# Performance work log

Measured on AMD Instinct MI355X. Metric: run time of the kernel, lower is better.

The kernel has to match this reference:

```python
import jax, jax.numpy as jnp
import numpy as np

IN_DIM = 1024
OUT_DIM = 1024
QK_DIM = OUT_DIM // 4  # 256


def setup_inputs() -> dict:
    key = jax.random.key(0)
    kx, ky, kq, kk, kv = jax.random.split(key, 5)
    B, Sq, Sk = 16, 2048, 2048
    x = jax.random.normal(kx, (B, Sq, IN_DIM), dtype=jnp.float32)
    y = jax.random.normal(ky, (B, Sk, IN_DIM), dtype=jnp.float32)
    s = 1.0 / np.sqrt(IN_DIM)
    Wq = jax.random.normal(kq, (IN_DIM, QK_DIM), dtype=jnp.float32) * s
    Wk = jax.random.normal(kk, (IN_DIM, QK_DIM), dtype=jnp.float32) * s
    Wv = jax.random.normal(kv, (IN_DIM, OUT_DIM), dtype=jnp.float32) * s
    return {"x": x, "y": y, "Wq": Wq, "Wk": Wk, "Wv": Wv}


def reference(x, y, Wq, Wk, Wv):
    # q: [B,Sq,dk], k: [B,Sk,dk]
    q = jnp.einsum("bsd,dk->bsk", x, Wq)
    k = jnp.einsum("btd,dk->btk", y, Wk)
    # NOTE: original scales by out_dim**0.5, not qk dim
    scores = jnp.einsum("bsk,btk->bst", q, k) / jnp.sqrt(jnp.float32(OUT_DIM))
    attn = jax.nn.softmax(scores, axis=-1)
    v = jnp.einsum("btd,de->bte", y, Wv)
    out = jnp.einsum("bst,bte->bse", attn, v)
    return out + x
```

## Files before the change

### kernel.cpp

```cpp
#include <hip/hip_runtime.h>

typedef __attribute__((ext_vector_type(8))) short bf16x8;
typedef __attribute__((ext_vector_type(4))) short s16x4;
typedef __attribute__((ext_vector_type(4))) float f32x4;

#define MFMA16(a,b,c) __builtin_amdgcn_mfma_f32_16x16x32_bf16((a),(b),(c),0,0,0)

__device__ __forceinline__ unsigned short f2bf(float f) {
  unsigned int u = __float_as_uint(f);
  return (unsigned short)((u + 0x7fffu + ((u >> 16) & 1u)) >> 16);
}
__device__ __forceinline__ float bf2f(unsigned short u) {
  return __uint_as_float(((unsigned int)u) << 16);
}

__device__ __forceinline__ void gload16(const void* g, void* l) {
  __builtin_amdgcn_global_load_lds((const __attribute__((address_space(1))) void*)g,
                                   (__attribute__((address_space(3))) void*)l, 16, 0, 0);
}

__global__ __launch_bounds__(256) void cvt_bf16(const float* __restrict__ in,
                                                unsigned short* __restrict__ out, int n8) {
  for (int i = blockIdx.x * 256 + threadIdx.x; i < n8; i += gridDim.x * 256) {
    float4 a = ((const float4*)in)[2 * i];
    float4 b = ((const float4*)in)[2 * i + 1];
    s16x4 p0, p1;
    p0[0] = f2bf(a.x); p0[1] = f2bf(a.y); p0[2] = f2bf(a.z); p0[3] = f2bf(a.w);
    p1[0] = f2bf(b.x); p1[1] = f2bf(b.y); p1[2] = f2bf(b.z); p1[3] = f2bf(b.w);
    ((s16x4*)out)[2 * i] = p0;
    ((s16x4*)out)[2 * i + 1] = p1;
  }
}

__global__ __launch_bounds__(256) void tcvt(const float* __restrict__ W,
                                            unsigned short* __restrict__ Wt, int K, int N) {
  __shared__ float t[32][33];
  const int n0 = blockIdx.x * 32, k0 = blockIdx.y * 32;
  const int c = threadIdx.x & 31, r8 = threadIdx.x >> 5;
#pragma unroll
  for (int p = 0; p < 4; ++p) {
    int r = r8 + p * 8;
    t[r][c] = W[(size_t)(k0 + r) * N + n0 + c];
  }
  __syncthreads();
#pragma unroll
  for (int p = 0; p < 4; ++p) {
    int r = r8 + p * 8;
    Wt[(size_t)(n0 + r) * K + k0 + c] = f2bf(t[c][r]);
  }
}

__global__ __launch_bounds__(256) void proj_gemm(
    const unsigned short* __restrict__ A, const unsigned short* __restrict__ Bt,
    unsigned short* __restrict__ C, int N, float scale)
{
  __shared__ __align__(16) unsigned short As[2][4096];
  __shared__ __align__(16) unsigned short Bs[2][4096];
  const int tid = threadIdx.x, lane = tid & 63, w = tid >> 6;
  const int wr = w >> 1, wc = w & 1;
  const int lrow = lane & 15, lg = lane >> 4;
  const size_t bm = (size_t)blockIdx.x * 128;
  const size_t bn = (size_t)blockIdx.y * 128;
  const int rl = lane >> 2, cq = lane & 3;

  auto stage = [&](int kt, int buf) {
#pragma unroll
    for (int u = 0; u < 2; ++u) {
      int row = w * 32 + u * 16 + rl;
      gload16(A  + (bm + row) * 1024 + kt * 32 + cq * 8, &As[buf][(w * 32 + u * 16) * 32]);
      gload16(Bt + (bn + row) * 1024 + kt * 32 + cq * 8, &Bs[buf][(w * 32 + u * 16) * 32]);
    }
  };

  f32x4 acc[4][4] = {};
  stage(0, 0);
  __syncthreads();

  for (int kt = 0; kt < 32; ++kt) {
    const int cur = kt & 1;
    if (kt + 1 < 32) stage(kt + 1, cur ^ 1);
    bf16x8 af[4], bfr[4];
#pragma unroll
    for (int i = 0; i < 4; ++i)
      af[i] = *(const bf16x8*)&As[cur][(wr * 64 + i * 16 + lrow) * 32 + lg * 8];
#pragma unroll
    for (int j = 0; j < 4; ++j)
      bfr[j] = *(const bf16x8*)&Bs[cur][(wc * 64 + j * 16 + lrow) * 32 + lg * 8];
    __builtin_amdgcn_s_setprio(1);
#pragma unroll
    for (int i = 0; i < 4; ++i)
#pragma unroll
      for (int j = 0; j < 4; ++j)
        acc[i][j] = MFMA16(af[i], bfr[j], acc[i][j]);
    __builtin_amdgcn_s_setprio(0);
    __syncthreads();
  }

  const int orow0 = blockIdx.x * 128 + wr * 64;
  const int ocol0 = blockIdx.y * 128 + wc * 64;
#pragma unroll
  for (int i = 0; i < 4; ++i)
#pragma unroll
    for (int j = 0; j < 4; ++j) {
      int col = ocol0 + j * 16 + lrow;
#pragma unroll
      for (int r = 0; r < 4; ++r) {
        int row = orow0 + i * 16 + lg * 4 + r;
        C[(size_t)row * N + col] = f2bf(acc[i][j][r] * scale);
      }
    }
}

#define SBAR  do { __builtin_amdgcn_s_barrier(); __builtin_amdgcn_sched_barrier(0); } while (0)

template<int NT, int NTIL, int MODE>
__global__ __launch_bounds__(512) void gemm4p(
    const unsigned short* __restrict__ Aall, const unsigned short* __restrict__ Ball,
    size_t abatch, size_t bbatch, int lda, int ldb,
    unsigned short* __restrict__ Cb, int b0, int nb)
{
  __shared__ __align__(16) unsigned short lds[65536];
  const int bid = blockIdx.x;
  const int bloc = bid % nb, tl = bid / nb;
  const int mtile = tl / NTIL, ntile = tl % NTIL;
  const int gb = b0 + bloc;
  const unsigned short* Ag = Aall + (MODE == 0 ? (size_t)gb : (size_t)bloc) * abatch
                                  + (size_t)mtile * 256 * lda;
  const unsigned short* Bg = Ball + (size_t)gb * bbatch + (size_t)ntile * 256 * ldb;

  const int tid = threadIdx.x, lane = tid & 63, w = tid >> 6;
  const int wm = w >> 2, wn = w & 3;
  const int lrow = lane & 15, lg = lane >> 4;
  char* lb = (char*)lds;

  auto stageU = [&](const unsigned short* G, int ld, int kofs, int ubyte) {
#pragma unroll
    for (int i = 0; i < 2; ++i) {
      int c = tid + 512 * i;
      int row = c >> 2, q = c & 3;
      int qs = q ^ ((row >> 1) & 3);
      gload16(G + (size_t)row * ld + kofs + qs * 8, lb + ubyte + c * 16);
    }
  };
  auto rdfrag = [&](int ubyte, int row) -> bf16x8 {
    return *(const bf16x8*)(lb + ubyte + row * 64 + ((lg ^ ((row >> 1) & 3)) << 4));
  };

  f32x4 acc[8][4] = {};
  bf16x8 afA[4], afB[4], bfrA[4], bfrB[4];

  stageU(Ag, lda, 0,  (0 * 2 + 0) * 16384);
  stageU(Bg, ldb, 0,  (1 * 2 + 0) * 16384);
  stageU(Ag, lda, 32, (2 * 2 + 0) * 16384);
  stageU(Bg, ldb, 32, (3 * 2 + 0) * 16384);
  stageU(Ag, lda, 64, (0 * 2 + 1) * 16384);
  stageU(Bg, ldb, 64, (1 * 2 + 1) * 16384);
  asm volatile("s_waitcnt vmcnt(8)" ::: "memory");
  SBAR;
#pragma unroll
  for (int i = 0; i < 4; ++i) afA[i] = rdfrag(0, wm * 128 + i * 16 + lrow);
#pragma unroll
  for (int nf = 0; nf < 4; ++nf) bfrA[nf] = rdfrag(2 * 16384, wn * 64 + nf * 16 + lrow);

  for (int T = 0; T < NT; ++T) {
    const int pc = T & 1, pn = (T + 1) & 1;
    const int a1b = (2 * 2 + pc) * 16384, b1b = (3 * 2 + pc) * 16384;
    const int a0b = (0 * 2 + pc) * 16384;
    const int t1 = (T + 1 < NT) ? T + 1 : 0;
    const int t2 = (T + 2 < NT) ? T + 2 : 0;

#pragma unroll
    for (int i = 0; i < 4; ++i) afB[i] = rdfrag(a0b, wm * 128 + (i + 4) * 16 + lrow);
    stageU(Ag, lda, t1 * 64 + 32, (2 * 2 + pn) * 16384);
    asm volatile("s_waitcnt lgkmcnt(4)" ::: "memory");
    __builtin_amdgcn_sched_barrier(0);
    __builtin_amdgcn_s_setprio(1);
#pragma unroll
    for (int mf = 0; mf < 4; ++mf)
#pragma unroll
      for (int nf = 0; nf < 4; ++nf)
        acc[mf][nf] = MFMA16(afA[mf], bfrA[nf], acc[mf][nf]);
    __builtin_amdgcn_s_setprio(0);
    asm volatile("s_waitcnt vmcnt(6)" ::: "memory");
    SBAR;

#pragma unroll
    for (int i = 0; i < 4; ++i) afA[i] = rdfrag(a1b, wm * 128 + i * 16 + lrow);
#pragma unroll
    for (int nf = 0; nf < 4; ++nf) bfrB[nf] = rdfrag(b1b, wn * 64 + nf * 16 + lrow);
    stageU(Bg, ldb, t1 * 64 + 32, (3 * 2 + pn) * 16384);
    asm volatile("s_waitcnt lgkmcnt(8)" ::: "memory");
    __builtin_amdgcn_sched_barrier(0);
    __builtin_amdgcn_s_setprio(1);
#pragma unroll
    for (int mf = 0; mf < 4; ++mf)
#pragma unroll
      for (int nf = 0; nf < 4; ++nf)
        acc[mf + 4][nf] = MFMA16(afB[mf], bfrA[nf], acc[mf + 4][nf]);
    __builtin_amdgcn_s_setprio(0);
    SBAR;

#pragma unroll
    for (int i = 0; i < 4; ++i) afB[i] = rdfrag(a1b, wm * 128 + (i + 4) * 16 + lrow);
    stageU(Ag, lda, t2 * 64, (0 * 2 + pc) * 16384);
    asm volatile("s_waitcnt lgkmcnt(4)" ::: "memory");
    __builtin_amdgcn_sched_barrier(0);
    __builtin_amdgcn_s_setprio(1);
#pragma unroll
    for (int mf = 0; mf < 4; ++mf)
#pragma unroll
      for (int nf = 0; nf < 4; ++nf)
        acc[mf][nf] = MFMA16(afA[mf], bfrB[nf], acc[mf][nf]);
    __builtin_amdgcn_s_setprio(0);
    asm volatile("s_waitcnt vmcnt(6)" ::: "memory");
    SBAR;

#pragma unroll
    for (int i = 0; i < 4; ++i) afA[i] = rdfrag((0 * 2 + pn) * 16384, wm * 128 + i * 16 + lrow);
#pragma unroll
    for (int nf = 0; nf < 4; ++nf) bfrA[nf] = rdfrag((1 * 2 + pn) * 16384, wn * 64 + nf * 16 + lrow);
    stageU(Bg, ldb, t2 * 64, (1 * 2 + pc) * 16384);
    asm volatile("s_waitcnt lgkmcnt(8)" ::: "memory");
    __builtin_amdgcn_sched_barrier(0);
    __builtin_amdgcn_s_setprio(1);
#pragma unroll
    for (int mf = 0; mf < 4; ++mf)
#pragma unroll
      for (int nf = 0; nf < 4; ++nf)
        acc[mf + 4][nf] = MFMA16(afB[mf], bfrB[nf], acc[mf + 4][nf]);
    __builtin_amdgcn_s_setprio(0);
    SBAR;
  }

  if (MODE == 0) {
    unsigned short* Cp = Cb + (size_t)bloc * 2048 * 2048;
#pragma unroll
    for (int mf = 0; mf < 8; ++mf)
#pragma unroll
      for (int r = 0; r < 4; ++r) {
        int row = mtile * 256 + wm * 128 + mf * 16 + lg * 4 + r;
#pragma unroll
        for (int nf = 0; nf < 4; ++nf) {
          int col = ntile * 256 + wn * 64 + nf * 16 + lrow;
          Cp[(size_t)row * 2048 + col] = f2bf(acc[mf][nf][r]);
        }
      }
  } else {
    unsigned char* C8 = (unsigned char*)Cb;
#pragma unroll
    for (int mf = 0; mf < 8; ++mf) {
      int m0 = mtile * 256 + wm * 128 + mf * 16 + lg * 4;
      int bb = m0 >> 11, t = m0 & 2047;
      int tw = t >> 6, t64 = t & 63;
#pragma unroll
      for (int nf = 0; nf < 4; ++nf) {
        int e = ntile * 256 + wn * 64 + nf * 16 + lrow;
        int eg = e >> 4;
        int pk = 0;
        pk = __builtin_amdgcn_cvt_pk_fp8_f32(acc[mf][nf][0], acc[mf][nf][1], pk, false);
        pk = __builtin_amdgcn_cvt_pk_fp8_f32(acc[mf][nf][2], acc[mf][nf][3], pk, true);
        *(unsigned int*)(C8 + (size_t)bb * 2097152
                            + ((size_t)(eg * 32 + tw)) * 1024 + lrow * 64 + t64)
            = (unsigned int)pk;
      }
    }
  }
}

__global__ __launch_bounds__(256) void softmax_kernel(
    const unsigned short* __restrict__ Sp, unsigned char* __restrict__ Pp) {
  const int row = blockIdx.x * 4 + (threadIdx.x >> 6);
  const int lane = threadIdx.x & 63;
  const unsigned short* rp = Sp + (size_t)row * 2048;
  bf16x8 raw[4];
#pragma unroll
  for (int c = 0; c < 4; ++c) raw[c] = *(const bf16x8*)(rp + c * 512 + lane * 8);
  float v[32];
#pragma unroll
  for (int c = 0; c < 4; ++c)
#pragma unroll
    for (int j = 0; j < 8; ++j) v[c * 8 + j] = bf2f((unsigned short)raw[c][j]);
  float mx = v[0];
#pragma unroll
  for (int j = 1; j < 32; ++j) mx = fmaxf(mx, v[j]);
  mx = fmaxf(mx, __shfl_xor(mx, 1));
  mx = fmaxf(mx, __shfl_xor(mx, 2));
  mx = fmaxf(mx, __shfl_xor(mx, 4));
  mx = fmaxf(mx, __shfl_xor(mx, 8));
  mx = fmaxf(mx, __shfl_xor(mx, 16));
  mx = fmaxf(mx, __shfl_xor(mx, 32));
  float sum = 0.f;
#pragma unroll
  for (int j = 0; j < 32; ++j) { v[j] = __expf(v[j] - mx); sum += v[j]; }
  sum += __shfl_xor(sum, 1);
  sum += __shfl_xor(sum, 2);
  sum += __shfl_xor(sum, 4);
  sum += __shfl_xor(sum, 8);
  sum += __shfl_xor(sum, 16);
  sum += __shfl_xor(sum, 32);
  const float scale = 64.0f / sum;
  unsigned char* rp8 = Pp + (size_t)row * 2048;
#pragma unroll
  for (int c = 0; c < 4; ++c) {
    int lo = 0, hi = 0;
    lo = __builtin_amdgcn_cvt_pk_fp8_f32(v[c * 8 + 0] * scale, v[c * 8 + 1] * scale, lo, false);
    lo = __builtin_amdgcn_cvt_pk_fp8_f32(v[c * 8 + 2] * scale, v[c * 8 + 3] * scale, lo, true);
    hi = __builtin_amdgcn_cvt_pk_fp8_f32(v[c * 8 + 4] * scale, v[c * 8 + 5] * scale, hi, false);
    hi = __builtin_amdgcn_cvt_pk_fp8_f32(v[c * 8 + 6] * scale, v[c * 8 + 7] * scale, hi, true);
    uint2 o; o.x = (unsigned int)lo; o.y = (unsigned int)hi;
    *(uint2*)(rp8 + c * 512 + lane * 8) = o;
  }
}

__global__ __launch_bounds__(512) void pvf8_kernel(
    const unsigned char* __restrict__ Pp,
    const unsigned char* __restrict__ Vp,
    const float* __restrict__ X, float* __restrict__ Out,
    int b0, int nb)
{
  __shared__ __align__(16) unsigned char lds[4][16384];
  const int bloc = blockIdx.x % nb, tl = blockIdx.x / nb;
  const int mtile = tl >> 3, ntile = tl & 7;
  const int gb = b0 + bloc;
  const unsigned char* Ag = Pp + (size_t)bloc * 4194304 + (size_t)mtile * 256 * 2048;
  const unsigned char* Vb = Vp + (size_t)gb * 2097152;
  const int NT = 32;
  const int tid = threadIdx.x, lane = tid & 63, w = tid >> 6;
  const int wm = w >> 2, wn = w & 3;
  const int lrow = lane & 15, lg = lane >> 4;

  auto stageA = [&](int jt) {
    unsigned char* dst = lds[jt & 3];
#pragma unroll
    for (int i = 0; i < 2; ++i) {
      int c = tid + 512 * i; int row = c >> 2; int q = (c & 3) ^ ((row >> 1) & 3);
      gload16(Ag + (size_t)row * 2048 + jt * 64 + q * 16, dst + c * 16);
    }
  };

  f32x4 acc[8][2] = {};
  stageA(0); stageA(1); stageA(2);
  asm volatile("s_waitcnt vmcnt(4)" ::: "memory");

  for (int jt = 0; jt < NT; ++jt) {
    __builtin_amdgcn_s_barrier();
    long2 bv[2];
#pragma unroll
    for (int nf = 0; nf < 2; ++nf) {
      int eg = ntile * 8 + wn * 2 + nf;
      bv[nf] = *(const long2*)(Vb + ((size_t)(eg * 32 + jt)) * 1024 + lrow * 64 + lg * 16);
    }
    if (jt + 3 < NT) stageA(jt + 3);
    const unsigned char* Ab = lds[jt & 3];
    {
      long2 av[4];
#pragma unroll
      for (int mf = 0; mf < 4; ++mf) {
        int row = wm * 128 + mf * 16 + lrow;
        av[mf] = *(const long2*)(Ab + row * 64 + ((lg ^ ((row >> 1) & 3)) << 4));
      }
      __builtin_amdgcn_s_setprio(1);
#pragma unroll
      for (int mf = 0; mf < 4; ++mf)
#pragma unroll
        for (int nf = 0; nf < 2; ++nf) {
          acc[mf][nf] = __builtin_amdgcn_mfma_f32_16x16x32_fp8_fp8(av[mf].x, bv[nf].x, acc[mf][nf], 0, 0, 0);
          acc[mf][nf] = __builtin_amdgcn_mfma_f32_16x16x32_fp8_fp8(av[mf].y, bv[nf].y, acc[mf][nf], 0, 0, 0);
        }
      __builtin_amdgcn_s_setprio(0);
    }
    {
      long2 av[4];
#pragma unroll
      for (int mf = 0; mf < 4; ++mf) {
        int row = wm * 128 + (mf + 4) * 16 + lrow;
        av[mf] = *(const long2*)(Ab + row * 64 + ((lg ^ ((row >> 1) & 3)) << 4));
      }
      __builtin_amdgcn_s_setprio(1);
#pragma unroll
      for (int mf = 0; mf < 4; ++mf)
#pragma unroll
        for (int nf = 0; nf < 2; ++nf) {
          acc[mf + 4][nf] = __builtin_amdgcn_mfma_f32_16x16x32_fp8_fp8(av[mf].x, bv[nf].x, acc[mf + 4][nf], 0, 0, 0);
          acc[mf + 4][nf] = __builtin_amdgcn_mfma_f32_16x16x32_fp8_fp8(av[mf].y, bv[nf].y, acc[mf + 4][nf], 0, 0, 0);
        }
      __builtin_amdgcn_s_setprio(0);
    }
  }

#pragma unroll
  for (int mf = 0; mf < 8; ++mf)
#pragma unroll
    for (int r = 0; r < 4; ++r) {
      int row = mtile * 256 + wm * 128 + mf * 16 + lg * 4 + r;
      const float* xr = X   + ((size_t)gb * 2048 + row) * 1024;
      float*      orp = Out + ((size_t)gb * 2048 + row) * 1024;
#pragma unroll
      for (int nf = 0; nf < 2; ++nf) {
        int col = ntile * 128 + wn * 32 + nf * 16 + lrow;
        orp[col] = acc[mf][nf][r] * 0.015625f + xr[col];
      }
    }
}

extern "C" void kernel_launch(void* const* d_in, const int* in_sizes, int n_in,
                              void* d_out, int out_size, void* d_ws, size_t ws_size,
                              hipStream_t stream) {
  (void)in_sizes; (void)n_in; (void)out_size;
  const float* x  = (const float*)d_in[0];
  const float* y  = (const float*)d_in[1];
  const float* Wq = (const float*)d_in[2];
  const float* Wk = (const float*)d_in[3];
  const float* Wv = (const float*)d_in[4];
  float* out = (float*)d_out;

  unsigned short* xb = (unsigned short*)d_out;
  unsigned short* yb = xb + (size_t)16 * 2048 * 1024;

  char* p = (char*)d_ws;
  unsigned short* Wqt = (unsigned short*)p;  p += (size_t)256 * 1024 * 2;
  unsigned short* Wkt = (unsigned short*)p;  p += (size_t)256 * 1024 * 2;
  unsigned short* Wvt = (unsigned short*)p;  p += (size_t)1024 * 1024 * 2;
  unsigned short* qws = (unsigned short*)p;  p += (size_t)16 * 2048 * 256 * 2;
  unsigned short* kws = (unsigned short*)p;  p += (size_t)16 * 2048 * 256 * 2;
  unsigned char*  vp8 = (unsigned char*)p;   p += (size_t)16 * 1024 * 2048;
  char* dyn = p;
  const size_t fixed_bytes = (size_t)(dyn - (char*)d_ws);
  const size_t per_batch = (size_t)2048 * 2048 * 2 + (size_t)2048 * 2048;
  int nb = 1;
  if      (ws_size >= fixed_bytes + 16 * per_batch) nb = 16;
  else if (ws_size >= fixed_bytes + 8  * per_batch) nb = 8;
  else if (ws_size >= fixed_bytes + 4  * per_batch) nb = 4;
  else if (ws_size >= fixed_bytes + 2  * per_batch) nb = 2;
  else nb = 1;
  unsigned short* Sp = (unsigned short*)dyn;
  unsigned char*  Pp = (unsigned char*)(dyn + (size_t)nb * 2048 * 2048 * 2);

  const int n8 = (16 * 2048 * 1024) / 8;
  cvt_bf16<<<2048, 256, 0, stream>>>(x, xb, n8);
  cvt_bf16<<<2048, 256, 0, stream>>>(y, yb, n8);
  tcvt<<<dim3(8, 32),  256, 0, stream>>>(Wq, Wqt, 1024, 256);
  tcvt<<<dim3(8, 32),  256, 0, stream>>>(Wk, Wkt, 1024, 256);
  tcvt<<<dim3(32, 32), 256, 0, stream>>>(Wv, Wvt, 1024, 1024);

  proj_gemm<<<dim3(256, 2), 256, 0, stream>>>(xb, Wqt, qws, 256, 0.03125f);
  proj_gemm<<<dim3(256, 2), 256, 0, stream>>>(yb, Wkt, kws, 256, 1.0f);
  gemm4p<16, 4, 2><<<512, 512, 0, stream>>>(
      yb, Wvt, 0, 0, 1024, 1024, (unsigned short*)vp8, 0, 1);

  for (int b0 = 0; b0 < 16; b0 += nb) {
    gemm4p<4, 8, 0><<<nb * 64, 512, 0, stream>>>(
        qws, kws, (size_t)2048 * 256, (size_t)2048 * 256, 256, 256,
        Sp, b0, nb);
    softmax_kernel<<<nb * 512, 256, 0, stream>>>(Sp, Pp);
    pvf8_kernel<<<nb * 64, 512, 0, stream>>>(Pp, vp8, x, out, b0, nb);
  }
}
```

Measured before the change: 460.3 us.

## Merge Q/K projections into one gemm4p launch and prefetch V fragments

The two separate 128x128 proj_gemm launches for Q and K are replaced by a single launch of the larger 256-tile gemm4p kernel with a new output mode. That mode writes bf16 results and applies the 1/32 scale only to the Q half. This relies on xb/yb, Wqt/Wkt and qws/kws being laid out back to back in the workspace. Separately, the P·V kernel now loads V register fragments one iteration ahead, so the global load latency overlaps with the MFMA work, at the cost of extra registers.

```diff
diff --git a/kernel.cpp b/kernel.cpp
--- a/kernel.cpp
+++ b/kernel.cpp
@@ -48,67 +48,6 @@
     int r = r8 + p * 8;
     Wt[(size_t)(n0 + r) * K + k0 + c] = f2bf(t[c][r]);
   }
-}
-
-__global__ __launch_bounds__(256) void proj_gemm(
-    const unsigned short* __restrict__ A, const unsigned short* __restrict__ Bt,
-    unsigned short* __restrict__ C, int N, float scale)
-{
-  __shared__ __align__(16) unsigned short As[2][4096];
-  __shared__ __align__(16) unsigned short Bs[2][4096];
-  const int tid = threadIdx.x, lane = tid & 63, w = tid >> 6;
-  const int wr = w >> 1, wc = w & 1;
-  const int lrow = lane & 15, lg = lane >> 4;
-  const size_t bm = (size_t)blockIdx.x * 128;
-  const size_t bn = (size_t)blockIdx.y * 128;
-  const int rl = lane >> 2, cq = lane & 3;
-
-  auto stage = [&](int kt, int buf) {
-#pragma unroll
-    for (int u = 0; u < 2; ++u) {
-      int row = w * 32 + u * 16 + rl;
-      gload16(A  + (bm + row) * 1024 + kt * 32 + cq * 8, &As[buf][(w * 32 + u * 16) * 32]);
-      gload16(Bt + (bn + row) * 1024 + kt * 32 + cq * 8, &Bs[buf][(w * 32 + u * 16) * 32]);
-    }
-  };
-
-  f32x4 acc[4][4] = {};
-  stage(0, 0);
-  __syncthreads();
-
-  for (int kt = 0; kt < 32; ++kt) {
-    const int cur = kt & 1;
-    if (kt + 1 < 32) stage(kt + 1, cur ^ 1);
-    bf16x8 af[4], bfr[4];
-#pragma unroll
-    for (int i = 0; i < 4; ++i)
-      af[i] = *(const bf16x8*)&As[cur][(wr * 64 + i * 16 + lrow) * 32 + lg * 8];
-#pragma unroll
-    for (int j = 0; j < 4; ++j)
-      bfr[j] = *(const bf16x8*)&Bs[cur][(wc * 64 + j * 16 + lrow) * 32 + lg * 8];
-    __builtin_amdgcn_s_setprio(1);
-#pragma unroll
-    for (int i = 0; i < 4; ++i)
-#pragma unroll
-      for (int j = 0; j < 4; ++j)
-        acc[i][j] = MFMA16(af[i], bfr[j], acc[i][j]);
-    __builtin_amdgcn_s_setprio(0);
-    __syncthreads();
-  }
-
-  const int orow0 = blockIdx.x * 128 + wr * 64;
-  const int ocol0 = blockIdx.y * 128 + wc * 64;
-#pragma unroll
-  for (int i = 0; i < 4; ++i)
-#pragma unroll
-    for (int j = 0; j < 4; ++j) {
-      int col = ocol0 + j * 16 + lrow;
-#pragma unroll
-      for (int r = 0; r < 4; ++r) {
-        int row = orow0 + i * 16 + lg * 4 + r;
-        C[(size_t)row * N + col] = f2bf(acc[i][j][r] * scale);
-      }
-    }
 }
 
 #define SBAR  do { __builtin_amdgcn_s_barrier(); __builtin_amdgcn_sched_barrier(0); } while (0)
@@ -245,7 +184,7 @@
           Cp[(size_t)row * 2048 + col] = f2bf(acc[mf][nf][r]);
         }
       }
-  } else {
+  } else if (MODE == 2) {
     unsigned char* C8 = (unsigned char*)Cb;
 #pragma unroll
     for (int mf = 0; mf < 8; ++mf) {
@@ -264,6 +203,20 @@
             = (unsigned int)pk;
       }
     }
+  } else {
+    unsigned short* Cp = Cb + (size_t)bloc * 16 * 2048 * 256;
+    const float scale = (bloc == 0) ? 0.03125f : 1.0f;
+#pragma unroll
+    for (int mf = 0; mf < 8; ++mf)
+#pragma unroll
+      for (int r = 0; r < 4; ++r) {
+        int row = mtile * 256 + wm * 128 + mf * 16 + lg * 4 + r;
+#pragma unroll
+        for (int nf = 0; nf < 4; ++nf) {
+          int col = wn * 64 + nf * 16 + lrow;
+          Cp[(size_t)row * 256 + col] = f2bf(acc[mf][nf][r] * scale);
+        }
+      }
   }
 }
 
@@ -337,20 +290,26 @@
       gload16(Ag + (size_t)row * 2048 + jt * 64 + q * 16, dst + c * 16);
     }
   };
-
-  f32x4 acc[8][2] = {};
-  stageA(0); stageA(1); stageA(2);
-  asm volatile("s_waitcnt vmcnt(4)" ::: "memory");
-
-  for (int jt = 0; jt < NT; ++jt) {
-    __builtin_amdgcn_s_barrier();
-    long2 bv[2];
+  auto loadB = [&](int jt, long2* bv) {
 #pragma unroll
     for (int nf = 0; nf < 2; ++nf) {
       int eg = ntile * 8 + wn * 2 + nf;
       bv[nf] = *(const long2*)(Vb + ((size_t)(eg * 32 + jt)) * 1024 + lrow * 64 + lg * 16);
     }
+  };
+
+  f32x4 acc[8][2] = {};
+  stageA(0); stageA(1); stageA(2);
+  long2 bvc[2];
+  loadB(0, bvc);
+  asm volatile("s_waitcnt vmcnt(6)" ::: "memory");
+  __builtin_amdgcn_sched_barrier(0);
+
+  for (int jt = 0; jt < NT; ++jt) {
+    __builtin_amdgcn_s_barrier();
     if (jt + 3 < NT) stageA(jt + 3);
+    long2 bvn[2];
+    loadB(jt + 1 < NT ? jt + 1 : 0, bvn);
     const unsigned char* Ab = lds[jt & 3];
     {
       long2 av[4];
@@ -364,8 +323,8 @@
       for (int mf = 0; mf < 4; ++mf)
 #pragma unroll
         for (int nf = 0; nf < 2; ++nf) {
-          acc[mf][nf] = __builtin_amdgcn_mfma_f32_16x16x32_fp8_fp8(av[mf].x, bv[nf].x, acc[mf][nf], 0, 0, 0);
-          acc[mf][nf] = __builtin_amdgcn_mfma_f32_16x16x32_fp8_fp8(av[mf].y, bv[nf].y, acc[mf][nf], 0, 0, 0);
+          acc[mf][nf] = __builtin_amdgcn_mfma_f32_16x16x32_fp8_fp8(av[mf].x, bvc[nf].x, acc[mf][nf], 0, 0, 0);
+          acc[mf][nf] = __builtin_amdgcn_mfma_f32_16x16x32_fp8_fp8(av[mf].y, bvc[nf].y, acc[mf][nf], 0, 0, 0);
         }
       __builtin_amdgcn_s_setprio(0);
     }
@@ -381,11 +340,12 @@
       for (int mf = 0; mf < 4; ++mf)
 #pragma unroll
         for (int nf = 0; nf < 2; ++nf) {
-          acc[mf + 4][nf] = __builtin_amdgcn_mfma_f32_16x16x32_fp8_fp8(av[mf].x, bv[nf].x, acc[mf + 4][nf], 0, 0, 0);
-          acc[mf + 4][nf] = __builtin_amdgcn_mfma_f32_16x16x32_fp8_fp8(av[mf].y, bv[nf].y, acc[mf + 4][nf], 0, 0, 0);
+          acc[mf + 4][nf] = __builtin_amdgcn_mfma_f32_16x16x32_fp8_fp8(av[mf].x, bvc[nf].x, acc[mf + 4][nf], 0, 0, 0);
+          acc[mf + 4][nf] = __builtin_amdgcn_mfma_f32_16x16x32_fp8_fp8(av[mf].y, bvc[nf].y, acc[mf + 4][nf], 0, 0, 0);
         }
       __builtin_amdgcn_s_setprio(0);
     }
+    bvc[0] = bvn[0]; bvc[1] = bvn[1];
   }
 
 #pragma unroll
@@ -443,8 +403,9 @@
   tcvt<<<dim3(8, 32),  256, 0, stream>>>(Wk, Wkt, 1024, 256);
   tcvt<<<dim3(32, 32), 256, 0, stream>>>(Wv, Wvt, 1024, 1024);
 
-  proj_gemm<<<dim3(256, 2), 256, 0, stream>>>(xb, Wqt, qws, 256, 0.03125f);
-  proj_gemm<<<dim3(256, 2), 256, 0, stream>>>(yb, Wkt, kws, 256, 1.0f);
+  gemm4p<16, 1, 3><<<256, 512, 0, stream>>>(
+      xb, Wqt, (size_t)16 * 2048 * 1024, (size_t)256 * 1024, 1024, 1024,
+      qws, 0, 2);
   gemm4p<16, 4, 2><<<512, 512, 0, stream>>>(
       yb, Wvt, 0, 0, 1024, 1024, (unsigned short*)vp8, 0, 1);
 
```

Measured after the change: 430.0 us. 6.6% less time.
